# Kernel tuning notes

Measured on AMD Instinct MI355X. Metric: run time of the kernel, lower is better.

Reference implementation:

```python
import jax, jax.numpy as jnp
import numpy as np

EMBED_DIM = 1024
NUM_HEADS = 16
NUM_KV_HEADS = 4
HEAD_DIM = 64
GQA_RATIO = NUM_HEADS // NUM_KV_HEADS
SCALE = 1.0 / np.sqrt(HEAD_DIM).astype(np.float32)
B, L = 1, 4096
NUM_SEQS = 8  # 8 packed sequences of length 512


def setup_inputs() -> dict:
    key = jax.random.key(0)
    k1, k2, k3, k4, k5 = jax.random.split(key, 5)
    hidden_states = jax.random.normal(k1, (B, L, EMBED_DIM), dtype=jnp.float32)
    cu_seqlens = (jnp.arange(NUM_SEQS + 1, dtype=jnp.int32) * (L // NUM_SEQS))
    s = 1.0 / np.sqrt(EMBED_DIM)
    Wq = jax.random.normal(k2, (EMBED_DIM, NUM_HEADS * HEAD_DIM), dtype=jnp.float32) * s
    Wk = jax.random.normal(k3, (EMBED_DIM, NUM_KV_HEADS * HEAD_DIM), dtype=jnp.float32) * s
    Wv = jax.random.normal(k4, (EMBED_DIM, NUM_KV_HEADS * HEAD_DIM), dtype=jnp.float32) * s
    Wo = jax.random.normal(k5, (NUM_HEADS * HEAD_DIM, EMBED_DIM), dtype=jnp.float32) * s
    return {"hidden_states": hidden_states, "Wq": Wq, "Wk": Wk, "Wv": Wv, "Wo": Wo,
            "cu_seqlens": cu_seqlens}


def reference(hidden_states, Wq, Wk, Wv, Wo, cu_seqlens):
    b, l, d = hidden_states.shape
    # QKV projections (Linear, no bias)
    q = (hidden_states @ Wq).reshape(b, l, NUM_HEADS, HEAD_DIM)
    k = (hidden_states @ Wk).reshape(b, l, NUM_KV_HEADS, HEAD_DIM)
    v = (hidden_states @ Wv).reshape(b, l, NUM_KV_HEADS, HEAD_DIM)
    # GQA: expand kv heads to num_heads (faithful to module's manual expand)
    k = jnp.repeat(k, GQA_RATIO, axis=2)  # [b, l, H, hd]
    v = jnp.repeat(v, GQA_RATIO, axis=2)
    # [b, H, l, hd]
    q = q.transpose(0, 2, 1, 3)
    k = k.transpose(0, 2, 1, 3)
    v = v.transpose(0, 2, 1, 3)
    # block-diagonal varlen mask from cu_seqlens
    pos = jnp.arange(l, dtype=jnp.int32)
    seq_ids = jnp.searchsorted(cu_seqlens, pos, side='right') - 1  # [l]
    mask = seq_ids[:, None] == seq_ids[None, :]                    # [l, l]
    # dense SDPA with mask
    scores = jnp.einsum('bhqd,bhkd->bhqk', q, k) * SCALE
    scores = jnp.where(mask[None, None], scores, jnp.finfo(scores.dtype).min)
    attn = jax.nn.softmax(scores, axis=-1)
    out = jnp.einsum('bhqk,bhkd->bhqd', attn, v)
    out = out.transpose(0, 2, 1, 3).reshape(b, l, NUM_HEADS * HEAD_DIM)
    return out @ Wo
```

## Files before the change

kernel.cpp:

```cpp
#include <hip/hip_runtime.h>
#include <hip/hip_bf16.h>
#include <stdint.h>
#include <stddef.h>

typedef __attribute__((ext_vector_type(8))) short short8;
typedef __attribute__((ext_vector_type(4))) short short4v;
typedef __attribute__((ext_vector_type(4))) float f32x4;

__device__ inline void store_c(float* p, float v) { *p = v; }
__device__ inline void store_c(__hip_bfloat16* p, float v) { *p = __float2bfloat16(v); }

__device__ __forceinline__ void gld_lds16(const __hip_bfloat16* g, __hip_bfloat16* l)
{
#if __has_builtin(__builtin_amdgcn_global_load_lds)
    __builtin_amdgcn_global_load_lds(
        (const __attribute__((address_space(1))) unsigned int*)g,
        (__attribute__((address_space(3))) unsigned int*)l,
        16, 0, 0);
#else
    *(short8*)((char*)l + (threadIdx.x & 63) * 16) = *(const short8*)g;
#endif
}

__global__ __launch_bounds__(256) void convert_kernel(const float* __restrict__ in,
                                                      __hip_bfloat16* __restrict__ out,
                                                      int n4)
{
    int i = blockIdx.x * blockDim.x + threadIdx.x;
    if (i >= n4) return;
    const f32x4 v = *(const f32x4*)(in + (size_t)i * 4);
    union { __hip_bfloat16 t[4]; short4v s4; } u;
    #pragma unroll
    for (int j = 0; j < 4; ++j) u.t[j] = __float2bfloat16(v[j]);
    *(short4v*)(out + (size_t)i * 4) = u.s4;
}

__global__ __launch_bounds__(256) void transpose_kernel(const float* __restrict__ Wq,
                                                        const float* __restrict__ Wk,
                                                        const float* __restrict__ Wv,
                                                        const float* __restrict__ Wo,
                                                        __hip_bfloat16* __restrict__ Wt)
{
    __shared__ float tile[32][33];
    const int bk = blockIdx.x;
    const int bn = blockIdx.y;
    const int tx = threadIdx.x & 31;
    const int ty = threadIdx.x >> 5;
    const int n0 = bn * 32;

    const float* src; int ld; int col0;
    if (n0 < 1024)      { src = Wq; ld = 1024; col0 = n0; }
    else if (n0 < 1280) { src = Wk; ld = 256;  col0 = n0 - 1024; }
    else if (n0 < 1536) { src = Wv; ld = 256;  col0 = n0 - 1280; }
    else                { src = Wo; ld = 1024; col0 = n0 - 1536; }

    #pragma unroll
    for (int r = 0; r < 4; ++r) {
        int k = ty + 8 * r;
        tile[k][tx] = src[(size_t)(bk * 32 + k) * ld + col0 + tx];
    }
    __syncthreads();
    #pragma unroll
    for (int r = 0; r < 4; ++r) {
        int nl = ty + 8 * r;
        Wt[(size_t)(n0 + nl) * 1024 + bk * 32 + tx] = __float2bfloat16(tile[tx][nl]);
    }
}

#define BK 32

template <int BM, int BN, typename CT>
__global__ __launch_bounds__(256) void gemm_gld_kernel(const __hip_bfloat16* __restrict__ A,
                                                       const __hip_bfloat16* __restrict__ Bt,
                                                       CT* __restrict__ C,
                                                       int M, int N, int K)
{
    constexpr int MF = BM / 32;
    constexpr int NF = BN / 32;
    __shared__ __align__(16) __hip_bfloat16 As[BM * BK];
    __shared__ __align__(16) __hip_bfloat16 Bs[BN * BK];

    const int tid  = threadIdx.x;
    const int lane = tid & 63;
    const int wave = tid >> 6;
    const int wm = wave >> 1;
    const int wn = wave & 1;
    const int fr = lane & 15;
    const int fk = (lane >> 4) * 8;

    const __hip_bfloat16* Ab = A  + (size_t)(blockIdx.x * BM) * K;
    const __hip_bfloat16* Bb = Bt + (size_t)(blockIdx.y * BN) * K;

    const int srow = lane >> 2;
    const int scol = (lane & 3) * 8;

    f32x4 acc[MF][NF];
    const f32x4 z4 = {0.f, 0.f, 0.f, 0.f};
    #pragma unroll
    for (int i = 0; i < MF; ++i)
        #pragma unroll
        for (int j = 0; j < NF; ++j) acc[i][j] = z4;

    for (int k0 = 0; k0 < K; k0 += BK) {
        for (int i = wave; i < BM / 16; i += 4)
            gld_lds16(Ab + (size_t)(i * 16 + srow) * K + k0 + scol, &As[i * 512]);
        for (int i = wave; i < BN / 16; i += 4)
            gld_lds16(Bb + (size_t)(i * 16 + srow) * K + k0 + scol, &Bs[i * 512]);
        __syncthreads();

        short8 af[MF], bfv[NF];
        #pragma unroll
        for (int mf = 0; mf < MF; ++mf)
            af[mf] = *(const short8*)&As[(wm * (BM / 2) + mf * 16 + fr) * BK + fk];
        #pragma unroll
        for (int nf = 0; nf < NF; ++nf)
            bfv[nf] = *(const short8*)&Bs[(wn * (BN / 2) + nf * 16 + fr) * BK + fk];
        #pragma unroll
        for (int mf = 0; mf < MF; ++mf)
            #pragma unroll
            for (int nf = 0; nf < NF; ++nf)
                acc[mf][nf] = __builtin_amdgcn_mfma_f32_16x16x32_bf16(af[mf], bfv[nf], acc[mf][nf], 0, 0, 0);
        __syncthreads();
    }

    const int crow = blockIdx.x * BM + wm * (BM / 2);
    const int ccol = blockIdx.y * BN + wn * (BN / 2);
    #pragma unroll
    for (int mf = 0; mf < MF; ++mf)
        #pragma unroll
        for (int nf = 0; nf < NF; ++nf)
            #pragma unroll
            for (int r = 0; r < 4; ++r) {
                int row = crow + mf * 16 + (lane >> 4) * 4 + r;
                int col = ccol + nf * 16 + fr;
                store_c(&C[(size_t)row * N + col], acc[mf][nf][r]);
            }
}

__global__ __launch_bounds__(256) void attn_kernel(const __hip_bfloat16* __restrict__ QKV,
                                                   __hip_bfloat16* __restrict__ O)
{
    __shared__ __align__(16) __hip_bfloat16 Ks[64][72];
    __shared__ __align__(16) __hip_bfloat16 Vts[64][72];
    __shared__ __align__(16) __hip_bfloat16 Ps[4][32][72];

    const int tid  = threadIdx.x;
    const int lane = tid & 63;
    const int wave = tid >> 6;
    const int qt = blockIdx.x;
    const int h  = blockIdx.y;
    const int sq = blockIdx.z;
    const int kvh = h >> 2;

    const int fr = lane & 15;
    const int fg = lane >> 4;
    const int fk = fg * 8;

    const int q0 = sq * 512 + qt * 128 + wave * 32;

    short8 qf[2][2];
    #pragma unroll
    for (int mf = 0; mf < 2; ++mf)
        #pragma unroll
        for (int kc = 0; kc < 2; ++kc)
            qf[mf][kc] = *(const short8*)(QKV + (size_t)(q0 + mf * 16 + fr) * 1536 + h * 64 + kc * 32 + fk);

    const f32x4 z4 = {0.f, 0.f, 0.f, 0.f};
    f32x4 acc_o[2][4];
    #pragma unroll
    for (int a = 0; a < 2; ++a)
        #pragma unroll
        for (int b = 0; b < 4; ++b) acc_o[a][b] = z4;

    float m_run[2][4], l_run[2][4];
    #pragma unroll
    for (int a = 0; a < 2; ++a)
        #pragma unroll
        for (int r = 0; r < 4; ++r) { m_run[a][r] = -1e30f; l_run[a][r] = 0.f; }

    const float cs = 0.125f * 1.44269504088896340736f;

    for (int t = 0; t < 8; ++t) {
        const int kvbase = sq * 512 + t * 64;

        #pragma unroll
        for (int i = 0; i < 2; ++i) {
            int cc = tid + 256 * i;
            int r = cc >> 3, dch = cc & 7;
            short8 v = *(const short8*)(QKV + (size_t)(kvbase + r) * 1536 + 1024 + kvh * 64 + dch * 8);
            *(short8*)&Ks[r][dch * 8] = v;
        }
        {
            const int kv = tid & 63;
            const int pos = (kv & 15) * 4 + (kv >> 4);
            #pragma unroll
            for (int i = 0; i < 2; ++i) {
                int dc = (tid >> 6) + 4 * i;
                short8 v = *(const short8*)(QKV + (size_t)(kvbase + kv) * 1536 + 1280 + kvh * 64 + dc * 8);
                #pragma unroll
                for (int b = 0; b < 8; ++b)
                    Vts[dc * 8 + b][pos] = ((const __hip_bfloat16*)&v)[b];
            }
        }
        __syncthreads();

        f32x4 s[2][4];
        #pragma unroll
        for (int a = 0; a < 2; ++a)
            #pragma unroll
            for (int b = 0; b < 4; ++b) s[a][b] = z4;
        #pragma unroll
        for (int nf = 0; nf < 4; ++nf) {
            short8 kf0 = *(const short8*)&Ks[nf * 16 + fr][fk];
            short8 kf1 = *(const short8*)&Ks[nf * 16 + fr][32 + fk];
            #pragma unroll
            for (int mf = 0; mf < 2; ++mf) {
                s[mf][nf] = __builtin_amdgcn_mfma_f32_16x16x32_bf16(qf[mf][0], kf0, s[mf][nf], 0, 0, 0);
                s[mf][nf] = __builtin_amdgcn_mfma_f32_16x16x32_bf16(qf[mf][1], kf1, s[mf][nf], 0, 0, 0);
            }
        }

        #pragma unroll
        for (int mf = 0; mf < 2; ++mf) {
            #pragma unroll
            for (int r = 0; r < 4; ++r) {
                float mx = fmaxf(fmaxf(s[mf][0][r], s[mf][1][r]), fmaxf(s[mf][2][r], s[mf][3][r]));
                #pragma unroll
                for (int off = 1; off < 16; off <<= 1)
                    mx = fmaxf(mx, __shfl_xor(mx, off));
                float mnew = fmaxf(m_run[mf][r], mx);
                float f = exp2f((m_run[mf][r] - mnew) * cs);
                m_run[mf][r] = mnew;
                float p0 = exp2f((s[mf][0][r] - mnew) * cs);
                float p1 = exp2f((s[mf][1][r] - mnew) * cs);
                float p2 = exp2f((s[mf][2][r] - mnew) * cs);
                float p3 = exp2f((s[mf][3][r] - mnew) * cs);
                l_run[mf][r] = l_run[mf][r] * f + (p0 + p1 + p2 + p3);
                #pragma unroll
                for (int nf = 0; nf < 4; ++nf)
                    acc_o[mf][nf][r] *= f;
                int rl = mf * 16 + fg * 4 + r;
                union { __hip_bfloat16 h[4]; short4v s4; } pw;
                pw.h[0] = __float2bfloat16(p0);
                pw.h[1] = __float2bfloat16(p1);
                pw.h[2] = __float2bfloat16(p2);
                pw.h[3] = __float2bfloat16(p3);
                *(short4v*)&Ps[wave][rl][fr * 4] = pw.s4;
            }
        }

        #pragma unroll
        for (int kc = 0; kc < 2; ++kc) {
            short8 pa[2];
            #pragma unroll
            for (int mf = 0; mf < 2; ++mf)
                pa[mf] = *(const short8*)&Ps[wave][mf * 16 + fr][kc * 32 + fk];
            #pragma unroll
            for (int nf = 0; nf < 4; ++nf) {
                short8 vf = *(const short8*)&Vts[nf * 16 + fr][kc * 32 + fk];
                #pragma unroll
                for (int mf = 0; mf < 2; ++mf)
                    acc_o[mf][nf] = __builtin_amdgcn_mfma_f32_16x16x32_bf16(pa[mf], vf, acc_o[mf][nf], 0, 0, 0);
            }
        }
        __syncthreads();
    }

    #pragma unroll
    for (int mf = 0; mf < 2; ++mf) {
        #pragma unroll
        for (int r = 0; r < 4; ++r) {
            float lsum = l_run[mf][r];
            #pragma unroll
            for (int off = 1; off < 16; off <<= 1)
                lsum += __shfl_xor(lsum, off);
            float inv_l = 1.0f / lsum;
            int row = q0 + mf * 16 + fg * 4 + r;
            #pragma unroll
            for (int nf = 0; nf < 4; ++nf)
                O[(size_t)row * 1024 + h * 64 + nf * 16 + fr] =
                    __float2bfloat16(acc_o[mf][nf][r] * inv_l);
        }
    }
}

extern "C" void kernel_launch(void* const* d_in, const int* in_sizes, int n_in,
                              void* d_out, int out_size, void* d_ws, size_t ws_size,
                              hipStream_t stream)
{
    const float* hs = (const float*)d_in[0];
    const float* Wq = (const float*)d_in[1];
    const float* Wk = (const float*)d_in[2];
    const float* Wv = (const float*)d_in[3];
    const float* Wo = (const float*)d_in[4];

    char* ws = (char*)d_ws;
    __hip_bfloat16* hsb  = (__hip_bfloat16*)(ws);
    __hip_bfloat16* Wt   = (__hip_bfloat16*)(ws + 8388608);
    __hip_bfloat16* QKV  = (__hip_bfloat16*)(ws + 13631488);
    __hip_bfloat16* AOut = (__hip_bfloat16*)(ws + 26214400);
    float* out = (float*)d_out;

    convert_kernel<<<4096, 256, 0, stream>>>(hs, hsb, 1048576);
    transpose_kernel<<<dim3(32, 80), 256, 0, stream>>>(Wq, Wk, Wv, Wo, Wt);
    gemm_gld_kernel<64, 128, __hip_bfloat16><<<dim3(64, 12), 256, 0, stream>>>(hsb, Wt, QKV, 4096, 1536, 1024);
    attn_kernel<<<dim3(4, 16, 8), 256, 0, stream>>>(QKV, AOut);
    gemm_gld_kernel<64, 128, float><<<dim3(64, 8), 256, 0, stream>>>(AOut, Wt + (size_t)1536 * 1024, out, 4096, 1024, 1024);
}
```

Measured before the change: 167.3 us.

## Pre-transpose V into a global buffer and read K/V fragments directly from global memory

Adds a separate kernel that writes V transposed (with the permuted key order the attention kernel expects) into a workspace buffer. The attention kernel no longer stages K and V through shared memory. Each wave loads its MFMA fragments directly from global memory, which removes both per-tile __syncthreads barriers and the scattered LDS transpose writes. In exchange there is an extra kernel launch and global round trip for V, and the K/V reads become uncoalesced 16-byte loads that must rely on the cache, since all four waves now read the same data.

```diff
diff --git a/kernel.cpp b/kernel.cpp
--- a/kernel.cpp
+++ b/kernel.cpp
@@ -67,6 +67,30 @@
     }
 }
 
+__global__ __launch_bounds__(256) void vt_kernel(const __hip_bfloat16* __restrict__ QKV,
+                                                 __hip_bfloat16* __restrict__ Vt)
+{
+    __shared__ __hip_bfloat16 tile[32][34];
+    const int j0 = blockIdx.x * 32;
+    const int c0 = blockIdx.y * 32;
+    const int tx = threadIdx.x & 31;
+    const int ty = threadIdx.x >> 5;
+
+    #pragma unroll
+    for (int r = 0; r < 4; ++r) {
+        int jl = ty + 8 * r;
+        int j = j0 + jl;
+        int srcrow = (j & ~63) + (j & 3) * 16 + ((j >> 2) & 15);
+        tile[jl][tx] = QKV[(size_t)srcrow * 1536 + 1280 + c0 + tx];
+    }
+    __syncthreads();
+    #pragma unroll
+    for (int r = 0; r < 4; ++r) {
+        int cl = ty + 8 * r;
+        Vt[(size_t)(c0 + cl) * 4096 + j0 + tx] = tile[tx][cl];
+    }
+}
+
 #define BK 32
 
 template <int BM, int BN, typename CT>
@@ -138,10 +162,9 @@
 }
 
 __global__ __launch_bounds__(256) void attn_kernel(const __hip_bfloat16* __restrict__ QKV,
+                                                   const __hip_bfloat16* __restrict__ Vt,
                                                    __hip_bfloat16* __restrict__ O)
 {
-    __shared__ __align__(16) __hip_bfloat16 Ks[64][72];
-    __shared__ __align__(16) __hip_bfloat16 Vts[64][72];
     __shared__ __align__(16) __hip_bfloat16 Ps[4][32][72];
 
     const int tid  = threadIdx.x;
@@ -183,41 +206,23 @@
     for (int t = 0; t < 8; ++t) {
         const int kvbase = sq * 512 + t * 64;
 
-        #pragma unroll
-        for (int i = 0; i < 2; ++i) {
-            int cc = tid + 256 * i;
-            int r = cc >> 3, dch = cc & 7;
-            short8 v = *(const short8*)(QKV + (size_t)(kvbase + r) * 1536 + 1024 + kvh * 64 + dch * 8);
-            *(short8*)&Ks[r][dch * 8] = v;
-        }
-        {
-            const int kv = tid & 63;
-            const int pos = (kv & 15) * 4 + (kv >> 4);
-            #pragma unroll
-            for (int i = 0; i < 2; ++i) {
-                int dc = (tid >> 6) + 4 * i;
-                short8 v = *(const short8*)(QKV + (size_t)(kvbase + kv) * 1536 + 1280 + kvh * 64 + dc * 8);
+        f32x4 s[2][4];
+        #pragma unroll
+        for (int a = 0; a < 2; ++a)
+            #pragma unroll
+            for (int b = 0; b < 4; ++b) s[a][b] = z4;
+        #pragma unroll
+        for (int kc = 0; kc < 2; ++kc) {
+            short8 kf[4];
+            #pragma unroll
+            for (int nf = 0; nf < 4; ++nf)
+                kf[nf] = *(const short8*)(QKV + (size_t)(kvbase + nf * 16 + fr) * 1536
+                                          + 1024 + kvh * 64 + kc * 32 + fk);
+            #pragma unroll
+            for (int nf = 0; nf < 4; ++nf)
                 #pragma unroll
-                for (int b = 0; b < 8; ++b)
-                    Vts[dc * 8 + b][pos] = ((const __hip_bfloat16*)&v)[b];
-            }
-        }
-        __syncthreads();
-
-        f32x4 s[2][4];
-        #pragma unroll
-        for (int a = 0; a < 2; ++a)
-            #pragma unroll
-            for (int b = 0; b < 4; ++b) s[a][b] = z4;
-        #pragma unroll
-        for (int nf = 0; nf < 4; ++nf) {
-            short8 kf0 = *(const short8*)&Ks[nf * 16 + fr][fk];
-            short8 kf1 = *(const short8*)&Ks[nf * 16 + fr][32 + fk];
-            #pragma unroll
-            for (int mf = 0; mf < 2; ++mf) {
-                s[mf][nf] = __builtin_amdgcn_mfma_f32_16x16x32_bf16(qf[mf][0], kf0, s[mf][nf], 0, 0, 0);
-                s[mf][nf] = __builtin_amdgcn_mfma_f32_16x16x32_bf16(qf[mf][1], kf1, s[mf][nf], 0, 0, 0);
-            }
+                for (int mf = 0; mf < 2; ++mf)
+                    s[mf][nf] = __builtin_amdgcn_mfma_f32_16x16x32_bf16(qf[mf][kc], kf[nf], s[mf][nf], 0, 0, 0);
         }
 
         #pragma unroll
@@ -257,13 +262,13 @@
                 pa[mf] = *(const short8*)&Ps[wave][mf * 16 + fr][kc * 32 + fk];
             #pragma unroll
             for (int nf = 0; nf < 4; ++nf) {
-                short8 vf = *(const short8*)&Vts[nf * 16 + fr][kc * 32 + fk];
+                short8 vf = *(const short8*)(Vt + (size_t)(kvh * 64 + nf * 16 + fr) * 4096
+                                             + kvbase + kc * 32 + fk);
                 #pragma unroll
                 for (int mf = 0; mf < 2; ++mf)
                     acc_o[mf][nf] = __builtin_amdgcn_mfma_f32_16x16x32_bf16(pa[mf], vf, acc_o[mf][nf], 0, 0, 0);
             }
         }
-        __syncthreads();
     }
 
     #pragma unroll
@@ -299,11 +304,13 @@
     __hip_bfloat16* Wt   = (__hip_bfloat16*)(ws + 8388608);
     __hip_bfloat16* QKV  = (__hip_bfloat16*)(ws + 13631488);
     __hip_bfloat16* AOut = (__hip_bfloat16*)(ws + 26214400);
+    __hip_bfloat16* Vt   = (__hip_bfloat16*)(ws + 34603008);
     float* out = (float*)d_out;
 
     convert_kernel<<<4096, 256, 0, stream>>>(hs, hsb, 1048576);
     transpose_kernel<<<dim3(32, 80), 256, 0, stream>>>(Wq, Wk, Wv, Wo, Wt);
     gemm_gld_kernel<64, 128, __hip_bfloat16><<<dim3(64, 12), 256, 0, stream>>>(hsb, Wt, QKV, 4096, 1536, 1024);
-    attn_kernel<<<dim3(4, 16, 8), 256, 0, stream>>>(QKV, AOut);
+    vt_kernel<<<dim3(128, 8), 256, 0, stream>>>(QKV, Vt);
+    attn_kernel<<<dim3(4, 16, 8), 256, 0, stream>>>(QKV, Vt, AOut);
     gemm_gld_kernel<64, 128, float><<<dim3(64, 8), 256, 0, stream>>>(AOut, Wt + (size_t)1536 * 1024, out, 4096, 1024, 1024);
 }
```

After: 173.4 us. 1.04x slower.
